# Kernel optimization log

Measured on AMD Instinct MI355X. Metric: run time of the kernel, lower is better.

Reference implementation:

```python
import jax, jax.numpy as jnp
import numpy as np

D_MODEL = 2048
N_HEADS = 16
KV_HEADS = 4
HEAD_DIM = D_MODEL // N_HEADS  # 128
GROUPS = N_HEADS // KV_HEADS   # 4
CLIP_QKV = 8.0
EPS = 1e-5
MAX_POS = 2048
ROPE_THETA = 10000.0


def _make_rope(max_pos, dim, theta):
    inv_freq = 1.0 / (theta ** (np.arange(0, dim, 2, dtype=np.float32) / dim))
    t = np.arange(max_pos, dtype=np.float32)
    freqs = np.outer(t, inv_freq)                      # [max_pos, dim/2]
    emb = np.concatenate([freqs, freqs], axis=-1)      # [max_pos, dim]
    return jnp.asarray(np.sin(emb)), jnp.asarray(np.cos(emb))


def setup_inputs() -> dict:
    key = jax.random.key(0)
    ks = jax.random.split(key, 6)
    B, S = 2, 2048
    hidden_states = jax.random.normal(ks[0], (B, S, D_MODEL), dtype=jnp.float32)
    attention_mask = jnp.ones((B, S), dtype=jnp.int32)
    position_ids = jnp.broadcast_to(jnp.arange(S, dtype=jnp.int32)[None, :], (B, S))
    init_std = 0.02
    qkv_out = D_MODEL + 2 * KV_HEADS * HEAD_DIM
    wqkv = jax.random.normal(ks[1], (D_MODEL, qkv_out), dtype=jnp.float32) * init_std
    w_out = jax.random.normal(ks[2], (D_MODEL, D_MODEL), dtype=jnp.float32) * init_std
    norm1_w = jnp.ones((D_MODEL,), dtype=jnp.float32)
    norm2_w = jnp.ones((D_MODEL,), dtype=jnp.float32)
    rope_sin, rope_cos = _make_rope(MAX_POS, HEAD_DIM, ROPE_THETA)
    return {
        'hidden_states': hidden_states,
        'attention_mask': attention_mask,
        'position_ids': position_ids,
        'wqkv': wqkv,
        'w_out': w_out,
        'norm1_w': norm1_w,
        'norm2_w': norm2_w,
        'rope_sin': rope_sin,
        'rope_cos': rope_cos,
    }


def _rmsnorm(x, w, eps=EPS):
    var = jnp.mean(jnp.square(x), axis=-1, keepdims=True)
    return (x * jax.lax.rsqrt(var + eps)) * w


def _rotate_half(x):
    h = x.shape[-1] // 2
    return jnp.concatenate([-x[..., h:], x[..., :h]], axis=-1)


def reference(hidden_states, attention_mask, position_ids, wqkv, w_out, norm1_w, norm2_w, rope_sin, rope_cos):
    B, S, _ = hidden_states.shape
    residual = hidden_states
    # pre-norm
    x = _rmsnorm(hidden_states, norm1_w)
    # fused QKV projection + clip
    qkv = jnp.clip(x @ wqkv, -CLIP_QKV, CLIP_QKV)
    q = qkv[..., :D_MODEL].reshape(B, S, N_HEADS, HEAD_DIM)
    kv_sz = KV_HEADS * HEAD_DIM
    k = qkv[..., D_MODEL:D_MODEL + kv_sz].reshape(B, S, KV_HEADS, HEAD_DIM)
    v = qkv[..., D_MODEL + kv_sz:].reshape(B, S, KV_HEADS, HEAD_DIM)
    # rotary embedding (bshd layout)
    sin = rope_sin[position_ids][:, :, None, :]  # [B,S,1,hd]
    cos = rope_cos[position_ids][:, :, None, :]
    q = q * cos + _rotate_half(q) * sin
    k = k * cos + _rotate_half(k) * sin
    # GQA head repeat
    k = jnp.repeat(k, GROUPS, axis=2)  # [B,S,H,hd]
    v = jnp.repeat(v, GROUPS, axis=2)
    # attention
    scale = 1.0 / jnp.sqrt(jnp.float32(HEAD_DIM))
    scores = jnp.einsum('bqhd,bkhd->bhqk', q, k) * scale
    causal = jnp.tril(jnp.ones((S, S), dtype=bool))
    mask = causal[None, None, :, :] & (attention_mask[:, None, None, :] > 0)
    scores = jnp.where(mask, scores, jnp.finfo(scores.dtype).min)
    probs = jax.nn.softmax(scores, axis=-1)
    attn = jnp.einsum('bhqk,bkhd->bqhd', probs, v).reshape(B, S, D_MODEL)
    attn = attn @ w_out
    # residual add (resid dropout deterministic -> identity) + post-norm
    hidden = residual + attn
    residual_out = hidden
    post = _rmsnorm(hidden, norm2_w)
    return residual_out, post
```

## Files before the change

kernel.cpp:

```cpp
#include <hip/hip_runtime.h>
#include <cstdint>
#include <cstddef>

#define D_MODEL 2048
#define SEQ     2048
#define NB      2
#define ROWS    4096
#define QKV_N   3072
#define NH      16
#define NKV     4
#define HD      128
#define EPSV    1e-5f
#define QPRE    (0.08838834764831845f * 1.4426950408889634f)

typedef unsigned short ushort_t;
typedef __attribute__((ext_vector_type(8))) short  short8;
typedef __attribute__((ext_vector_type(4))) short  short4v;
typedef __attribute__((ext_vector_type(4))) float  floatx4;

__device__ __forceinline__ ushort_t f2b(float f) {
    unsigned u = __float_as_uint(f);
    u += 0x7fffu + ((u >> 16) & 1u);
    return (ushort_t)(u >> 16);
}
__device__ __forceinline__ float b2f(ushort_t u) {
    return __uint_as_float(((unsigned)u) << 16);
}

__device__ __forceinline__ unsigned pkbf(float lo, float hi) {
    unsigned u0 = __float_as_uint(lo) + 0x8000u;
    unsigned u1 = __float_as_uint(hi) + 0x8000u;
    return __builtin_amdgcn_perm(u1, u0, 0x07060302u);
}

#if __has_builtin(__builtin_amdgcn_mfma_f32_16x16x16bf16_1k)
#define HAVE_1K 1
#endif

__device__ __forceinline__ floatx4 pv_mfma(short4v a, short4v b, floatx4 c) {
#ifdef HAVE_1K
    return __builtin_amdgcn_mfma_f32_16x16x16bf16_1k(a, b, c, 0, 0, 0);
#else
    short8 a8 = {a[0], a[1], a[2], a[3], 0, 0, 0, 0};
    short8 b8 = {b[0], b[1], b[2], b[3], 0, 0, 0, 0};
    return __builtin_amdgcn_mfma_f32_16x16x32_bf16(a8, b8, c, 0, 0, 0);
#endif
}

#define GLD_LDS16(gp, lp) __builtin_amdgcn_global_load_lds( \
    (const __attribute__((address_space(1))) void*)(gp),   \
    (__attribute__((address_space(3))) void*)(lp), 16, 0, 0)

__global__ __launch_bounds__(256) void k_rmsnorm_bf16(
        const float* __restrict__ x, const float* __restrict__ w,
        ushort_t* __restrict__ out) {
    int row = blockIdx.x, t = threadIdx.x;
    const float4* xr = (const float4*)(x + (size_t)row * D_MODEL);
    float4 a = xr[t], b = xr[t + 256];
    float ss = a.x*a.x + a.y*a.y + a.z*a.z + a.w*a.w
             + b.x*b.x + b.y*b.y + b.z*b.z + b.w*b.w;
    for (int m = 1; m < 64; m <<= 1) ss += __shfl_xor(ss, m);
    __shared__ float sred[4];
    if ((t & 63) == 0) sred[t >> 6] = ss;
    __syncthreads();
    float r = rsqrtf((sred[0] + sred[1] + sred[2] + sred[3]) * (1.0f / D_MODEL) + EPSV);
    const float4* wr = (const float4*)w;
    float4 wa = wr[t], wb = wr[t + 256];
    ushort4 pa, pb;
    pa.x = f2b(a.x * r * wa.x); pa.y = f2b(a.y * r * wa.y);
    pa.z = f2b(a.z * r * wa.z); pa.w = f2b(a.w * r * wa.w);
    pb.x = f2b(b.x * r * wb.x); pb.y = f2b(b.y * r * wb.y);
    pb.z = f2b(b.z * r * wb.z); pb.w = f2b(b.w * r * wb.w);
    ushort4* o = (ushort4*)(out + (size_t)row * D_MODEL);
    o[t] = pa; o[t + 256] = pb;
}

__global__ __launch_bounds__(256) void k_rmsnorm_f32(
        const float* __restrict__ x, const float* __restrict__ w,
        float* __restrict__ out) {
    int row = blockIdx.x, t = threadIdx.x;
    const float4* xr = (const float4*)(x + (size_t)row * D_MODEL);
    float4 a = xr[t], b = xr[t + 256];
    float ss = a.x*a.x + a.y*a.y + a.z*a.z + a.w*a.w
             + b.x*b.x + b.y*b.y + b.z*b.z + b.w*b.w;
    for (int m = 1; m < 64; m <<= 1) ss += __shfl_xor(ss, m);
    __shared__ float sred[4];
    if ((t & 63) == 0) sred[t >> 6] = ss;
    __syncthreads();
    float r = rsqrtf((sred[0] + sred[1] + sred[2] + sred[3]) * (1.0f / D_MODEL) + EPSV);
    const float4* wr = (const float4*)w;
    float4 wa = wr[t], wb = wr[t + 256];
    float4 oa, ob;
    oa.x = a.x * r * wa.x; oa.y = a.y * r * wa.y; oa.z = a.z * r * wa.z; oa.w = a.w * r * wa.w;
    ob.x = b.x * r * wb.x; ob.y = b.y * r * wb.y; ob.z = b.z * r * wb.z; ob.w = b.w * r * wb.w;
    float4* o = (float4*)(out + (size_t)row * D_MODEL);
    o[t] = oa; o[t + 256] = ob;
}

__global__ __launch_bounds__(256) void k_transpose_cvt(
        const float* __restrict__ in, ushort_t* __restrict__ out, int R, int C) {
    __shared__ float tile[32][33];
    int bc = blockIdx.x * 32, br = blockIdx.y * 32;
    int t = threadIdx.x, lr = t >> 5, lc = t & 31;
    for (int i = 0; i < 4; i++)
        tile[lr + i * 8][lc] = in[(size_t)(br + lr + i * 8) * C + bc + lc];
    __syncthreads();
    for (int i = 0; i < 4; i++)
        out[(size_t)(bc + lr + i * 8) * R + br + lc] = f2b(tile[lc][lr + i * 8]);
}

template <int MODE>
__global__ __launch_bounds__(256) void k_gemm(
        const ushort_t* __restrict__ A, const ushort_t* __restrict__ Bt,
        void* __restrict__ Cout, const float* __restrict__ resid,
        int M, int N, int K) {
    __shared__ __align__(16) ushort_t sA[128 * 64];
    __shared__ __align__(16) ushort_t sB[128 * 64];
    int bm = blockIdx.y * 128, bn = blockIdx.x * 128;
    int t = threadIdx.x;
    int wv = t >> 6, lane = t & 63;
    int wm = (wv >> 1) * 64, wn = (wv & 1) * 64;
    int q4 = lane >> 4, n16 = lane & 15;

    int srow8 = lane >> 3;
    int sxor  = ((lane & 7) ^ srow8) * 8;
    const ushort_t* gA = A  + (size_t)(bm + wv * 32 + srow8) * K + sxor;
    const ushort_t* gB = Bt + (size_t)(bn + wv * 32 + srow8) * K + sxor;
    ushort_t* lA = sA + wv * 32 * 64;
    ushort_t* lB = sB + wv * 32 * 64;

    floatx4 zero4 = {0.0f, 0.0f, 0.0f, 0.0f};
    floatx4 acc[4][4];
    for (int i = 0; i < 4; i++)
        for (int j = 0; j < 4; j++) acc[i][j] = zero4;

    for (int k0 = 0; k0 < K; k0 += 64) {
        #pragma unroll
        for (int i = 0; i < 4; i++) {
            GLD_LDS16(gA + (size_t)(i * 8) * K + k0, lA + i * 8 * 64);
            GLD_LDS16(gB + (size_t)(i * 8) * K + k0, lB + i * 8 * 64);
        }
        __syncthreads();
        #pragma unroll
        for (int kk = 0; kk < 2; kk++) {
            short8 af[4], bfr[4];
            for (int i = 0; i < 4; i++) {
                int row = wm + i * 16 + n16;
                af[i]  = *(const short8*)&sA[row * 64 + (((kk * 4 + q4) ^ (row & 7)) * 8)];
            }
            for (int j = 0; j < 4; j++) {
                int row = wn + j * 16 + n16;
                bfr[j] = *(const short8*)&sB[row * 64 + (((kk * 4 + q4) ^ (row & 7)) * 8)];
            }
            for (int i = 0; i < 4; i++)
                for (int j = 0; j < 4; j++)
                    acc[i][j] = __builtin_amdgcn_mfma_f32_16x16x32_bf16(af[i], bfr[j], acc[i][j], 0, 0, 0);
        }
        __syncthreads();
    }

    for (int i = 0; i < 4; i++) {
        int rbase = bm + wm + i * 16 + q4 * 4;
        for (int j = 0; j < 4; j++) {
            int col = bn + wn + j * 16 + n16;
            if (MODE == 0) {
                ushort_t* C = (ushort_t*)Cout;
                for (int r = 0; r < 4; r++) {
                    float v = acc[i][j][r];
                    v = fminf(fmaxf(v, -8.0f), 8.0f);
                    C[(size_t)(rbase + r) * N + col] = f2b(v);
                }
            } else {
                float* C = (float*)Cout;
                for (int r = 0; r < 4; r++) {
                    float v = acc[i][j][r] + resid[(size_t)(rbase + r) * N + col];
                    C[(size_t)(rbase + r) * N + col] = v;
                }
            }
        }
    }
}

__global__ __launch_bounds__(256) void k_rope(
        const ushort_t* __restrict__ qkv, const int* __restrict__ pos_ids,
        const float* __restrict__ rsin, const float* __restrict__ rcos,
        ushort_t* __restrict__ qout, ushort_t* __restrict__ kout) {
    int wid  = blockIdx.x * 4 + (threadIdx.x >> 6);
    int lane = threadIdx.x & 63;
    int row = wid / 20, slot = wid - row * 20;
    int b = row >> 11, s = row & 2047;
    int pos = pos_ids[row];
    int col0 = (slot < 16) ? slot * HD : D_MODEL + (slot - 16) * HD;
    const ushort_t* src = qkv + (size_t)row * QKV_N + col0;
    float xl = b2f(src[lane]);
    float xh = b2f(src[lane + 64]);
    const float* cp = rcos + (size_t)pos * HD;
    const float* sp = rsin + (size_t)pos * HD;
    float cl = cp[lane], sl = sp[lane];
    float ch = cp[lane + 64], sh = sp[lane + 64];
    float mul = (slot < 16) ? QPRE : 1.0f;
    float ol = (xl * cl - xh * sl) * mul;
    float oh = (xh * ch + xl * sh) * mul;
    if (slot < 16) {
        size_t dst = ((size_t)(b * NH + slot) * SEQ + s) * HD;
        qout[dst + lane] = f2b(ol); qout[dst + lane + 64] = f2b(oh);
    } else {
        size_t dst = ((size_t)(b * NKV + (slot - 16)) * SEQ + s) * HD;
        kout[dst + lane] = f2b(ol); kout[dst + lane + 64] = f2b(oh);
    }
}

__global__ __launch_bounds__(256) void k_vtrans(
        const ushort_t* __restrict__ qkv, ushort_t* __restrict__ vt) {
    __shared__ ushort_t tile[32][33];
    int bh = blockIdx.z;
    int b = bh >> 2, h = bh & 3;
    int s0 = blockIdx.x * 32, d0 = blockIdx.y * 32;
    int t = threadIdx.x, lr = t >> 5, lc = t & 31;
    int col0 = D_MODEL + NKV * HD + h * HD;
    for (int i = 0; i < 4; i++)
        tile[lr + i * 8][lc] =
            qkv[((size_t)b * SEQ + s0 + lr + i * 8) * QKV_N + col0 + d0 + lc];
    __syncthreads();
    for (int i = 0; i < 4; i++)
        vt[((size_t)bh * HD + d0 + lr + i * 8) * SEQ + s0 + lc] = tile[lc][lr + i * 8];
}

__global__ __launch_bounds__(256, 2) void k_attn(
        const ushort_t* __restrict__ Q, const ushort_t* __restrict__ Kr,
        const ushort_t* __restrict__ Vt, const int* __restrict__ amask,
        ushort_t* __restrict__ O) {
    int bidx = blockIdx.x;
    int qt = (SEQ / 64 - 1) - (bidx >> 5);
    int bh = bidx & 31, h = bh & 15, b = bh >> 4;
    int wave = threadIdx.x >> 6, lane = threadIdx.x & 63;
    int q4 = lane >> 4, n16 = lane & 15;

    __shared__ __align__(16) ushort_t sK[2][64 * 128];
    __shared__ __align__(16) ushort_t sV[2][128 * 64];

    const ushort_t* Qh = Q  + (size_t)bh * SEQ * HD;
    const ushort_t* Kh = Kr + (size_t)(b * NKV + (h >> 2)) * SEQ * HD;
    const ushort_t* Vh = Vt + (size_t)(b * NKV + (h >> 2)) * HD * SEQ;
    const int* am = amask + b * SEQ;

    int q0 = qt * 64 + wave * 16;
    int qcol = q0 + n16;

    short8 qf[4];
    for (int kk = 0; kk < 4; kk++)
        qf[kk] = *(const short8*)(Qh + (size_t)qcol * HD + kk * 32 + q4 * 8);

    floatx4 zero4 = {0.0f, 0.0f, 0.0f, 0.0f};
    floatx4 o_acc[8];
    for (int dt = 0; dt < 8; dt++) o_acc[dt] = zero4;
    float m_i = -INFINITY, l_i = 0.0f;

    int krow_l = (lane >> 4);
    int kc_l   = lane & 15;
    int vrow_l = (lane >> 3);
    int vc_l   = lane & 7;

    auto stage_kv = [&](int buf, int kv0) {
        #pragma unroll
        for (int t = 0; t < 4; t++) {
            int krow = wave * 16 + t * 4 + krow_l;
            int kc   = kc_l ^ (krow & 7);
            GLD_LDS16(Kh + (size_t)(kv0 + krow) * HD + kc * 8,
                      &sK[buf][(wave * 16 + t * 4) * 128]);
            int vrow = wave * 32 + t * 8 + vrow_l;
            int vc   = vc_l ^ (vrow & 7);
            GLD_LDS16(Vh + (size_t)vrow * SEQ + kv0 + vc * 8,
                      &sV[buf][(wave * 32 + t * 8) * 64]);
        }
    };

    int kv_iters = qt + 1;

    stage_kv(0, 0);
    asm volatile("s_waitcnt vmcnt(0)" ::: "memory");
    __builtin_amdgcn_s_barrier();
    __builtin_amdgcn_sched_barrier(0);

    for (int it = 0; it < kv_iters; it++) {
        int cur = it & 1;
        int kv0 = it * 64;
        if (it + 1 < kv_iters)
            stage_kv(cur ^ 1, kv0 + 64);

        const ushort_t* sKc = sK[cur];
        const ushort_t* sVc = sV[cur];

        bool tail = (kv0 + 63 > q0);
        floatx4 st[4];
        for (int jj = 0; jj < 4; jj++) st[jj] = zero4;
        for (int jj = 0; jj < 4; jj++) {
            int krow = jj * 16 + n16;
            int sw = krow & 7;
            const ushort_t* kb = sKc + krow * 128;
            for (int kk = 0; kk < 4; kk++) {
                short8 kf = *(const short8*)(kb + ((kk * 4 + q4) ^ sw) * 8);
                st[jj] = __builtin_amdgcn_mfma_f32_16x16x32_bf16(kf, qf[kk], st[jj], 0, 0, 0);
            }
        }
        for (int jj = 0; jj < 4; jj++) {
            int kvb = kv0 + jj * 16 + q4 * 4;
            int4 am4 = *(const int4*)(am + kvb);
            int amr[4] = {am4.x, am4.y, am4.z, am4.w};
            if (tail) {
                for (int r = 0; r < 4; r++)
                    st[jj][r] = (amr[r] > 0 && kvb + r <= qcol) ? st[jj][r] : -1e30f;
            } else {
                for (int r = 0; r < 4; r++)
                    st[jj][r] = (amr[r] > 0) ? st[jj][r] : -1e30f;
            }
        }
        float mx = st[0][0];
        for (int jj = 0; jj < 4; jj++)
            for (int r = 0; r < 4; r++) mx = fmaxf(mx, st[jj][r]);
        mx = fmaxf(mx, __shfl_xor(mx, 16));
        mx = fmaxf(mx, __shfl_xor(mx, 32));
        if (!__all(mx - m_i <= 8.0f)) {
            float mnew = fmaxf(m_i, mx);
            float al = exp2f(m_i - mnew);
            m_i = mnew;
            l_i *= al;
            for (int dt = 0; dt < 8; dt++)
                o_acc[dt] *= al;
        }
        float rs = 0.0f;
        for (int jj = 0; jj < 4; jj++)
            for (int r = 0; r < 4; r++) {
                float p = exp2f(st[jj][r] - m_i);
                st[jj][r] = p;
                rs += p;
            }
        rs += __shfl_xor(rs, 16);
        rs += __shfl_xor(rs, 32);
        l_i += rs;
        for (int jj = 0; jj < 4; jj++) {
            union { unsigned u[2]; short4v s; } uu;
            uu.u[0] = pkbf(st[jj][0], st[jj][1]);
            uu.u[1] = pkbf(st[jj][2], st[jj][3]);
            short4v pfr = uu.s;
            int ch = jj * 2 + (q4 >> 1), hh = q4 & 1;
            for (int dt = 0; dt < 8; dt++) {
                int vrow = dt * 16 + n16;
                short4v vf = *(const short4v*)(sVc + vrow * 64 + ((ch ^ (vrow & 7)) * 8) + hh * 4);
                o_acc[dt] = pv_mfma(vf, pfr, o_acc[dt]);
            }
        }
        asm volatile("s_waitcnt vmcnt(0)" ::: "memory");
        __builtin_amdgcn_s_barrier();
        __builtin_amdgcn_sched_barrier(0);
    }
    float inv = 1.0f / l_i;
    ushort_t* orow = O + ((size_t)(b * SEQ) + qcol) * D_MODEL + h * HD + q4 * 4;
    for (int dt = 0; dt < 8; dt++) {
        uint2 pk;
        pk.x = pkbf(o_acc[dt][0] * inv, o_acc[dt][1] * inv);
        pk.y = pkbf(o_acc[dt][2] * inv, o_acc[dt][3] * inv);
        *(uint2*)(orow + dt * 16) = pk;
    }
}

extern "C" void kernel_launch(void* const* d_in, const int* in_sizes, int n_in,
                              void* d_out, int out_size, void* d_ws, size_t ws_size,
                              hipStream_t stream) {
    const float* hidden = (const float*)d_in[0];
    const int*   amask  = (const int*)d_in[1];
    const int*   pos    = (const int*)d_in[2];
    const float* wqkv   = (const float*)d_in[3];
    const float* wout   = (const float*)d_in[4];
    const float* n1w    = (const float*)d_in[5];
    const float* n2w    = (const float*)d_in[6];
    const float* rsin   = (const float*)d_in[7];
    const float* rcos   = (const float*)d_in[8];
    float* out0 = (float*)d_out;
    float* out1 = out0 + (size_t)ROWS * D_MODEL;

    char* ws = (char*)d_ws;
    ushort_t* x_bf    = (ushort_t*)ws;  ws += (size_t)ROWS * D_MODEL * 2;
    ushort_t* wqkv_t  = (ushort_t*)ws;  ws += (size_t)QKV_N * D_MODEL * 2;
    ushort_t* wout_t  = (ushort_t*)ws;  ws += (size_t)D_MODEL * D_MODEL * 2;
    ushort_t* qkv     = (ushort_t*)ws;  ws += (size_t)ROWS * QKV_N * 2;
    ushort_t* qrot    = (ushort_t*)ws;  ws += (size_t)NB * NH * SEQ * HD * 2;
    ushort_t* krot    = (ushort_t*)ws;  ws += (size_t)NB * NKV * SEQ * HD * 2;
    ushort_t* vt      = (ushort_t*)ws;  ws += (size_t)NB * NKV * HD * SEQ * 2;
    ushort_t* attn    = (ushort_t*)ws;  ws += (size_t)ROWS * D_MODEL * 2;

    k_rmsnorm_bf16<<<ROWS, 256, 0, stream>>>(hidden, n1w, x_bf);
    k_transpose_cvt<<<dim3(QKV_N / 32, D_MODEL / 32), 256, 0, stream>>>(wqkv, wqkv_t, D_MODEL, QKV_N);
    k_transpose_cvt<<<dim3(D_MODEL / 32, D_MODEL / 32), 256, 0, stream>>>(wout, wout_t, D_MODEL, D_MODEL);
    k_gemm<0><<<dim3(QKV_N / 128, ROWS / 128), 256, 0, stream>>>(x_bf, wqkv_t, qkv, nullptr, ROWS, QKV_N, D_MODEL);
    k_rope<<<ROWS * 20 / 4, 256, 0, stream>>>(qkv, pos, rsin, rcos, qrot, krot);
    k_vtrans<<<dim3(SEQ / 32, HD / 32, NB * NKV), 256, 0, stream>>>(qkv, vt);
    k_attn<<<(SEQ / 64) * 32, 256, 0, stream>>>(qrot, krot, vt, amask, attn);
    k_gemm<1><<<dim3(D_MODEL / 128, ROWS / 128), 256, 0, stream>>>(attn, wout_t, out0, hidden, ROWS, D_MODEL, D_MODEL);
    k_rmsnorm_f32<<<ROWS, 256, 0, stream>>>(out0, n2w, out1);
}
```

Before: 379.7 us.

## Use 32x32x16 MFMA in attention and pair causal q-tiles per block

Rewrites the attention kernel to use 32x32x16 bf16 MFMA instructions, with each wave owning 32 query rows. P fragments are rearranged across half-waves with lane shuffles so they can feed the PV MFMA. Each block now handles two 64-row query tiles, one from the front and one from the back of the causal range, so every block does the same amount of work. Half the blocks are launched, and waves whose query rows end before the current KV tile skip its compute. The goals are higher MFMA efficiency and better causal load balance, at the cost of more registers, a shared K/V load loop that runs for the longer tile, and idle waves during its later iterations.

```diff
diff --git a/kernel.cpp b/kernel.cpp
--- a/kernel.cpp
+++ b/kernel.cpp
@@ -14,9 +14,9 @@
 #define QPRE    (0.08838834764831845f * 1.4426950408889634f)
 
 typedef unsigned short ushort_t;
-typedef __attribute__((ext_vector_type(8))) short  short8;
-typedef __attribute__((ext_vector_type(4))) short  short4v;
-typedef __attribute__((ext_vector_type(4))) float  floatx4;
+typedef __attribute__((ext_vector_type(8)))  short short8;
+typedef __attribute__((ext_vector_type(4)))  float floatx4;
+typedef __attribute__((ext_vector_type(16))) float floatx16;
 
 __device__ __forceinline__ ushort_t f2b(float f) {
     unsigned u = __float_as_uint(f);
@@ -33,18 +33,12 @@
     return __builtin_amdgcn_perm(u1, u0, 0x07060302u);
 }
 
-#if __has_builtin(__builtin_amdgcn_mfma_f32_16x16x16bf16_1k)
-#define HAVE_1K 1
-#endif
-
-__device__ __forceinline__ floatx4 pv_mfma(short4v a, short4v b, floatx4 c) {
-#ifdef HAVE_1K
-    return __builtin_amdgcn_mfma_f32_16x16x16bf16_1k(a, b, c, 0, 0, 0);
-#else
-    short8 a8 = {a[0], a[1], a[2], a[3], 0, 0, 0, 0};
-    short8 b8 = {b[0], b[1], b[2], b[3], 0, 0, 0, 0};
-    return __builtin_amdgcn_mfma_f32_16x16x32_bf16(a8, b8, c, 0, 0, 0);
-#endif
+__device__ __forceinline__ void swap2(unsigned a, unsigned b, int hi,
+                                      unsigned &x, unsigned &y) {
+    unsigned ta = __shfl_xor(a, 32);
+    unsigned tb = __shfl_xor(b, 32);
+    x = hi ? tb : a;
+    y = hi ? b : ta;
 }
 
 #define GLD_LDS16(gp, lp) __builtin_amdgcn_global_load_lds( \
@@ -231,10 +225,10 @@
         const ushort_t* __restrict__ Vt, const int* __restrict__ amask,
         ushort_t* __restrict__ O) {
     int bidx = blockIdx.x;
-    int qt = (SEQ / 64 - 1) - (bidx >> 5);
+    int p = bidx >> 5;
     int bh = bidx & 31, h = bh & 15, b = bh >> 4;
     int wave = threadIdx.x >> 6, lane = threadIdx.x & 63;
-    int q4 = lane >> 4, n16 = lane & 15;
+    int q32 = lane & 31, hi = lane >> 5;
 
     __shared__ __align__(16) ushort_t sK[2][64 * 128];
     __shared__ __align__(16) ushort_t sV[2][128 * 64];
@@ -244,16 +238,19 @@
     const ushort_t* Vh = Vt + (size_t)(b * NKV + (h >> 2)) * HD * SEQ;
     const int* am = amask + b * SEQ;
 
-    int q0 = qt * 64 + wave * 16;
-    int qcol = q0 + n16;
-
-    short8 qf[4];
-    for (int kk = 0; kk < 4; kk++)
-        qf[kk] = *(const short8*)(Qh + (size_t)qcol * HD + kk * 32 + q4 * 8);
-
-    floatx4 zero4 = {0.0f, 0.0f, 0.0f, 0.0f};
-    floatx4 o_acc[8];
-    for (int dt = 0; dt < 8; dt++) o_acc[dt] = zero4;
+    int ph = 31 - p;
+    int qb = (wave < 2) ? (p * 64 + wave * 32) : (ph * 64 + (wave - 2) * 32);
+    int qcol = qb + q32;
+
+    short8 qf[8];
+    #pragma unroll
+    for (int kk = 0; kk < 8; kk++)
+        qf[kk] = *(const short8*)(Qh + (size_t)qcol * HD + kk * 16 + hi * 8);
+
+    const floatx16 zero16 = {0,0,0,0, 0,0,0,0, 0,0,0,0, 0,0,0,0};
+    floatx16 o_acc[4];
+    #pragma unroll
+    for (int dt = 0; dt < 4; dt++) o_acc[dt] = zero16;
     float m_i = -INFINITY, l_i = 0.0f;
 
     int krow_l = (lane >> 4);
@@ -275,7 +272,7 @@
         }
     };
 
-    int kv_iters = qt + 1;
+    int kv_iters = 32 - p;
 
     stage_kv(0, 0);
     asm volatile("s_waitcnt vmcnt(0)" ::: "memory");
@@ -291,63 +288,89 @@
         const ushort_t* sKc = sK[cur];
         const ushort_t* sVc = sV[cur];
 
-        bool tail = (kv0 + 63 > q0);
-        floatx4 st[4];
-        for (int jj = 0; jj < 4; jj++) st[jj] = zero4;
-        for (int jj = 0; jj < 4; jj++) {
-            int krow = jj * 16 + n16;
-            int sw = krow & 7;
-            const ushort_t* kb = sKc + krow * 128;
-            for (int kk = 0; kk < 4; kk++) {
-                short8 kf = *(const short8*)(kb + ((kk * 4 + q4) ^ sw) * 8);
-                st[jj] = __builtin_amdgcn_mfma_f32_16x16x32_bf16(kf, qf[kk], st[jj], 0, 0, 0);
-            }
-        }
-        for (int jj = 0; jj < 4; jj++) {
-            int kvb = kv0 + jj * 16 + q4 * 4;
-            int4 am4 = *(const int4*)(am + kvb);
-            int amr[4] = {am4.x, am4.y, am4.z, am4.w};
-            if (tail) {
-                for (int r = 0; r < 4; r++)
-                    st[jj][r] = (amr[r] > 0 && kvb + r <= qcol) ? st[jj][r] : -1e30f;
-            } else {
-                for (int r = 0; r < 4; r++)
-                    st[jj][r] = (amr[r] > 0) ? st[jj][r] : -1e30f;
-            }
-        }
-        float mx = st[0][0];
-        for (int jj = 0; jj < 4; jj++)
-            for (int r = 0; r < 4; r++) mx = fmaxf(mx, st[jj][r]);
-        mx = fmaxf(mx, __shfl_xor(mx, 16));
-        mx = fmaxf(mx, __shfl_xor(mx, 32));
-        if (!__all(mx - m_i <= 8.0f)) {
-            float mnew = fmaxf(m_i, mx);
-            float al = exp2f(m_i - mnew);
-            m_i = mnew;
-            l_i *= al;
-            for (int dt = 0; dt < 8; dt++)
-                o_acc[dt] *= al;
-        }
-        float rs = 0.0f;
-        for (int jj = 0; jj < 4; jj++)
-            for (int r = 0; r < 4; r++) {
-                float p = exp2f(st[jj][r] - m_i);
-                st[jj][r] = p;
-                rs += p;
-            }
-        rs += __shfl_xor(rs, 16);
-        rs += __shfl_xor(rs, 32);
-        l_i += rs;
-        for (int jj = 0; jj < 4; jj++) {
-            union { unsigned u[2]; short4v s; } uu;
-            uu.u[0] = pkbf(st[jj][0], st[jj][1]);
-            uu.u[1] = pkbf(st[jj][2], st[jj][3]);
-            short4v pfr = uu.s;
-            int ch = jj * 2 + (q4 >> 1), hh = q4 & 1;
-            for (int dt = 0; dt < 8; dt++) {
-                int vrow = dt * 16 + n16;
-                short4v vf = *(const short4v*)(sVc + vrow * 64 + ((ch ^ (vrow & 7)) * 8) + hh * 4);
-                o_acc[dt] = pv_mfma(vf, pfr, o_acc[dt]);
+        if (kv0 <= qb + 31) {
+            bool tail = (kv0 + 63 > qb);
+            floatx16 st[2];
+            st[0] = zero16; st[1] = zero16;
+            #pragma unroll
+            for (int half = 0; half < 2; half++) {
+                int krow = half * 32 + q32;
+                int sw = krow & 7;
+                const ushort_t* kb = sKc + krow * 128;
+                #pragma unroll
+                for (int kk = 0; kk < 8; kk++) {
+                    short8 kf = *(const short8*)(kb + (((2 * kk + hi) ^ sw) * 8));
+                    st[half] = __builtin_amdgcn_mfma_f32_32x32x16_bf16(kf, qf[kk], st[half], 0, 0, 0);
+                }
+            }
+            #pragma unroll
+            for (int half = 0; half < 2; half++) {
+                #pragma unroll
+                for (int g = 0; g < 4; g++) {
+                    int kvb = kv0 + half * 32 + 8 * g + 4 * hi;
+                    int4 am4 = *(const int4*)(am + kvb);
+                    int amr[4] = {am4.x, am4.y, am4.z, am4.w};
+                    #pragma unroll
+                    for (int r2 = 0; r2 < 4; r2++) {
+                        bool ok = (amr[r2] > 0) && (!tail || (kvb + r2 <= qcol));
+                        st[half][g * 4 + r2] = ok ? st[half][g * 4 + r2] : -1e30f;
+                    }
+                }
+            }
+            float mx = -INFINITY;
+            #pragma unroll
+            for (int half = 0; half < 2; half++)
+                #pragma unroll
+                for (int r = 0; r < 16; r++) mx = fmaxf(mx, st[half][r]);
+            mx = fmaxf(mx, __shfl_xor(mx, 32));
+            if (!__all(mx - m_i <= 8.0f)) {
+                float mnew = fmaxf(m_i, mx);
+                float al = exp2f(m_i - mnew);
+                m_i = mnew;
+                l_i *= al;
+                #pragma unroll
+                for (int dt = 0; dt < 4; dt++) o_acc[dt] *= al;
+            }
+            float rs = 0.0f;
+            #pragma unroll
+            for (int half = 0; half < 2; half++)
+                #pragma unroll
+                for (int r = 0; r < 16; r++) {
+                    float pv = exp2f(st[half][r] - m_i);
+                    st[half][r] = pv;
+                    rs += pv;
+                }
+            rs += __shfl_xor(rs, 32);
+            l_i += rs;
+            #pragma unroll
+            for (int half = 0; half < 2; half++) {
+                unsigned pk01 = pkbf(st[half][0],  st[half][1]);
+                unsigned pk23 = pkbf(st[half][2],  st[half][3]);
+                unsigned pk45 = pkbf(st[half][4],  st[half][5]);
+                unsigned pk67 = pkbf(st[half][6],  st[half][7]);
+                unsigned pk89 = pkbf(st[half][8],  st[half][9]);
+                unsigned pkab = pkbf(st[half][10], st[half][11]);
+                unsigned pkcd = pkbf(st[half][12], st[half][13]);
+                unsigned pkef = pkbf(st[half][14], st[half][15]);
+                unsigned w0, w1, w2, w3;
+                union { unsigned u[4]; short8 s; } f0, f1;
+                swap2(pk01, pk45, hi, w0, w2);
+                swap2(pk23, pk67, hi, w1, w3);
+                f0.u[0] = w0; f0.u[1] = w1; f0.u[2] = w2; f0.u[3] = w3;
+                swap2(pk89, pkcd, hi, w0, w2);
+                swap2(pkab, pkef, hi, w1, w3);
+                f1.u[0] = w0; f1.u[1] = w1; f1.u[2] = w2; f1.u[3] = w3;
+                #pragma unroll
+                for (int ks = 0; ks < 2; ks++) {
+                    short8 pf = ks ? f1.s : f0.s;
+                    int cg = (half * 2 + ks) * 2 + hi;
+                    #pragma unroll
+                    for (int dt = 0; dt < 4; dt++) {
+                        int vrow = dt * 32 + q32;
+                        short8 vf = *(const short8*)(sVc + vrow * 64 + ((cg ^ (vrow & 7)) * 8));
+                        o_acc[dt] = __builtin_amdgcn_mfma_f32_32x32x16_bf16(vf, pf, o_acc[dt], 0, 0, 0);
+                    }
+                }
             }
         }
         asm volatile("s_waitcnt vmcnt(0)" ::: "memory");
@@ -355,13 +378,16 @@
         __builtin_amdgcn_sched_barrier(0);
     }
     float inv = 1.0f / l_i;
-    ushort_t* orow = O + ((size_t)(b * SEQ) + qcol) * D_MODEL + h * HD + q4 * 4;
-    for (int dt = 0; dt < 8; dt++) {
-        uint2 pk;
-        pk.x = pkbf(o_acc[dt][0] * inv, o_acc[dt][1] * inv);
-        pk.y = pkbf(o_acc[dt][2] * inv, o_acc[dt][3] * inv);
-        *(uint2*)(orow + dt * 16) = pk;
-    }
+    ushort_t* orow = O + ((size_t)(b * SEQ) + qcol) * D_MODEL + h * HD;
+    #pragma unroll
+    for (int dt = 0; dt < 4; dt++)
+        #pragma unroll
+        for (int g = 0; g < 4; g++) {
+            uint2 pk;
+            pk.x = pkbf(o_acc[dt][4 * g]     * inv, o_acc[dt][4 * g + 1] * inv);
+            pk.y = pkbf(o_acc[dt][4 * g + 2] * inv, o_acc[dt][4 * g + 3] * inv);
+            *(uint2*)(orow + dt * 32 + 8 * g + 4 * hi) = pk;
+        }
 }
 
 extern "C" void kernel_launch(void* const* d_in, const int* in_sizes, int n_in,
@@ -395,7 +421,7 @@
     k_gemm<0><<<dim3(QKV_N / 128, ROWS / 128), 256, 0, stream>>>(x_bf, wqkv_t, qkv, nullptr, ROWS, QKV_N, D_MODEL);
     k_rope<<<ROWS * 20 / 4, 256, 0, stream>>>(qkv, pos, rsin, rcos, qrot, krot);
     k_vtrans<<<dim3(SEQ / 32, HD / 32, NB * NKV), 256, 0, stream>>>(qkv, vt);
-    k_attn<<<(SEQ / 64) * 32, 256, 0, stream>>>(qrot, krot, vt, amask, attn);
+    k_attn<<<16 * 32, 256, 0, stream>>>(qrot, krot, vt, amask, attn);
     k_gemm<1><<<dim3(D_MODEL / 128, ROWS / 128), 256, 0, stream>>>(attn, wout_t, out0, hidden, ROWS, D_MODEL, D_MODEL);
     k_rmsnorm_f32<<<ROWS, 256, 0, stream>>>(out0, n2w, out1);
 }
```

Result: no change. 385.4 us (+1.5%).
